# Kernel optimization log

Measured on AMD Instinct MI355X. Metric: run time of the kernel, lower is better.

## Reference

```python
import jax, jax.numpy as jnp
import numpy as np

B, C, H, W = 16, 256, 56, 56
HEADS, DHEAD = 8, 32
INNER = HEADS * DHEAD  # == C
BLOCK, HALO = 7, 3
WIN = BLOCK + 2 * HALO      # 13
REL = WIN                   # rel_size = block + 2*halo
HIDDEN = 4 * C
EPS = 1e-6
LS_INIT = 1e-6


def layernorm2d(x, w, b):
    # channels-first LayerNorm over C, x: (B,C,H,W)
    u = jnp.mean(x, axis=1, keepdims=True)
    s = jnp.mean((x - u) ** 2, axis=1, keepdims=True)
    xn = (x - u) * jax.lax.rsqrt(s + EPS)
    return w[None, :, None, None] * xn + b[None, :, None, None]


def rel_to_abs(x):
    # x: (b, l, 2r-1) -> (b, l, r)
    b, l, m = x.shape
    r = (m + 1) // 2
    x = jnp.pad(x, ((0, 0), (0, 0), (0, 1))).reshape(b, l * (m + 1))
    x = jnp.pad(x, ((0, 0), (0, m - l))).reshape(b, l + 1, m)
    return x[:, :l, -r:]


def relative_logits_1d(q, rel_k):
    # q: (b, h, w, d); rel_k: (2r-1, d) -> (b, h, r, w, r)
    b, h, w, _ = q.shape
    r = (rel_k.shape[0] + 1) // 2
    logits = jnp.einsum('bxyd,rd->bxyr', q, rel_k)
    logits = rel_to_abs(logits.reshape(b * h, w, -1)).reshape(b, h, w, r)
    return jnp.broadcast_to(logits[:, :, None], (b, h, r, w, r))


def rel_pos_bias(q, rel_h, rel_w):
    b = q.shape[0]
    r = (rel_w.shape[0] + 1) // 2
    q2 = q.reshape(b, BLOCK, BLOCK, DHEAD)
    lw = relative_logits_1d(q2, rel_w)                        # (b, x, i, y, j)
    lw = lw.transpose(0, 1, 3, 2, 4).reshape(b, BLOCK * BLOCK, r * r)
    lh = relative_logits_1d(q2.transpose(0, 2, 1, 3), rel_h)  # (b, y, i, x, j)
    lh = lh.transpose(0, 3, 1, 4, 2).reshape(b, BLOCK * BLOCK, r * r)
    return lw + lh


def halo_attention(x, wq, wkv, wo, bo, rel_h, rel_w):
    Bq, _, Hh, Ww = x.shape
    nh, nw = Hh // BLOCK, Ww // BLOCK
    nb = nh * nw
    # queries: non-overlapping blocks -> (B*nb, BLOCK^2, C)
    q_inp = x.reshape(Bq, C, nh, BLOCK, nw, BLOCK).transpose(0, 2, 4, 3, 5, 1)
    q_inp = q_inp.reshape(Bq * nb, BLOCK * BLOCK, C)
    # keys/values: overlapping haloed windows (like F.unfold with padding=HALO)
    xp = jnp.pad(x, ((0, 0), (0, 0), (HALO, HALO), (HALO, HALO)))
    rows = (jnp.arange(nh) * BLOCK)[:, None] + jnp.arange(WIN)
    cols = (jnp.arange(nw) * BLOCK)[:, None] + jnp.arange(WIN)
    kv = xp[:, :, rows][:, :, :, :, cols]
    kv = kv.transpose(0, 2, 4, 3, 5, 1).reshape(Bq * nb, WIN * WIN, C)
    q = q_inp @ wq.T
    k, v = jnp.split(kv @ wkv.T, 2, axis=-1)

    def split_heads(t):
        b2, n2, _ = t.shape
        return t.reshape(b2, n2, HEADS, DHEAD).transpose(0, 2, 1, 3).reshape(b2 * HEADS, n2, DHEAD)

    q, k, v = map(split_heads, (q, k, v))
    q = q * (DHEAD ** -0.5)
    sim = jnp.einsum('bid,bjd->bij', q, k) + rel_pos_bias(q, rel_h, rel_w)
    # mask out-of-bounds (zero-padded) halo positions
    onep = jnp.pad(jnp.ones((Hh, Ww), sim.dtype), ((HALO, HALO), (HALO, HALO)))
    m = (onep[rows][:, :, cols].transpose(0, 2, 1, 3).reshape(nb, WIN * WIN)) > 0
    sim = sim.reshape(Bq, nb, HEADS, BLOCK * BLOCK, WIN * WIN)
    sim = jnp.where(m[None, :, None, None, :], sim, -jnp.finfo(sim.dtype).max)
    sim = sim.reshape(Bq * nb * HEADS, BLOCK * BLOCK, WIN * WIN)
    attn = jax.nn.softmax(sim, axis=-1)
    out = jnp.einsum('bij,bjd->bid', attn, v)
    out = out.reshape(Bq * nb, HEADS, BLOCK * BLOCK, DHEAD).transpose(0, 2, 1, 3)
    out = out.reshape(Bq * nb, BLOCK * BLOCK, INNER) @ wo.T + bo
    out = out.reshape(Bq, nh, nw, BLOCK, BLOCK, C).transpose(0, 5, 1, 3, 2, 4)
    return out.reshape(Bq, C, Hh, Ww)


def _forward(x, ln1_w, ln1_b, ln2_w, ln2_b, wq, wkv, wo, bo, rel_h, rel_w,
             gamma1, gamma2, fc1_w, fc1_b, fc2_w, fc2_b):
    y = halo_attention(layernorm2d(x, ln1_w, ln1_b), wq, wkv, wo, bo, rel_h, rel_w)
    x = x + gamma1 * y  # drop_path = 0 -> identity
    z = layernorm2d(x, ln2_w, ln2_b).transpose(0, 2, 3, 1)  # NHWC
    z = jax.nn.gelu(z @ fc1_w.T + fc1_b, approximate=False)
    z = z @ fc2_w.T + fc2_b
    z = gamma2 * z
    return x + z.transpose(0, 3, 1, 2)


def setup_inputs() -> dict:
    key = jax.random.key(0)
    ks = jax.random.split(key, 8)
    n = lambda k, sh: jax.random.normal(k, sh, jnp.float32) * 0.02
    scale = DHEAD ** -0.5
    return dict(
        x=jax.random.normal(ks[0], (B, C, H, W), jnp.float32),
        ln1_w=jnp.ones((C,), jnp.float32), ln1_b=jnp.zeros((C,), jnp.float32),
        ln2_w=jnp.ones((C,), jnp.float32), ln2_b=jnp.zeros((C,), jnp.float32),
        wq=n(ks[1], (INNER, C)),
        wkv=n(ks[2], (2 * INNER, C)),
        wo=n(ks[3], (C, INNER)), bo=jnp.zeros((C,), jnp.float32),
        rel_h=jax.random.normal(ks[4], (2 * REL - 1, DHEAD), jnp.float32) * scale,
        rel_w=jax.random.normal(ks[5], (2 * REL - 1, DHEAD), jnp.float32) * scale,
        gamma1=jnp.full((1, C, 1, 1), LS_INIT, jnp.float32),
        gamma2=jnp.full((1, 1, 1, C), LS_INIT, jnp.float32),
        fc1_w=n(ks[6], (HIDDEN, C)), fc1_b=jnp.zeros((HIDDEN,), jnp.float32),
        fc2_w=n(ks[7], (C, HIDDEN)), fc2_b=jnp.zeros((C,), jnp.float32),
    )


def reference(x, ln1_w, ln1_b, ln2_w, ln2_b, wq, wkv, wo, bo, rel_h, rel_w,
              gamma1, gamma2, fc1_w, fc1_b, fc2_w, fc2_b):
    return _forward(x, ln1_w, ln1_b, ln2_w, ln2_b, wq, wkv, wo, bo, rel_h, rel_w,
                    gamma1, gamma2, fc1_w, fc1_b, fc2_w, fc2_b)
```

## Files before the change

### kernel.cpp

```cpp
#include <hip/hip_runtime.h>
#include <cmath>

#define DI __device__ __forceinline__

typedef unsigned short ushort_t;
typedef __attribute__((ext_vector_type(8))) short short8;
typedef __attribute__((ext_vector_type(8))) unsigned short ushort8;
typedef __attribute__((ext_vector_type(4))) unsigned short ushort4_t;
typedef __attribute__((ext_vector_type(4))) float floatx4;
typedef unsigned int u32;
typedef __attribute__((ext_vector_type(4))) u32 uintx4;

DI float bf2f(ushort_t u) {
    unsigned v = ((unsigned)u) << 16;
    float f;
    __builtin_memcpy(&f, &v, 4);
    return f;
}
DI ushort_t f2bf(float f) {
    unsigned u;
    __builtin_memcpy(&u, &f, 4);
    unsigned r = (u + 0x7FFFu + ((u >> 16) & 1u)) >> 16;
    return (ushort_t)r;
}
DI ushort_t f2bf_tr(float f) {
    unsigned u;
    __builtin_memcpy(&u, &f, 4);
    return (ushort_t)(u >> 16);
}
DI u32 pack2bf(float lo, float hi) {
    u32 a, b;
    __builtin_memcpy(&a, &lo, 4);
    __builtin_memcpy(&b, &hi, 4);
    return (a >> 16) | (b & 0xFFFF0000u);
}

DI void async_copy16(const ushort_t* gsrc, ushort_t* ldst) {
    auto gp = (const __attribute__((address_space(1))) u32*)gsrc;
    auto lp = (__attribute__((address_space(3))) u32*)ldst;
    __builtin_amdgcn_global_load_lds(gp, lp, 16, 0, 0);
}


__global__ void convert_all_kernel(const float* __restrict__ wq, const float* __restrict__ wkv,
                                   const float* __restrict__ wo, const float* __restrict__ fc1w,
                                   const float* __restrict__ fc2w, const float* __restrict__ relh,
                                   const float* __restrict__ relw,
                                   ushort_t* __restrict__ bqkv, ushort_t* __restrict__ woC,
                                   ushort_t* __restrict__ fc1C, ushort_t* __restrict__ fc2C,
                                   ushort_t* __restrict__ relC, ushort_t* __restrict__ boneB) {
    int i = blockIdx.x * 256 + threadIdx.x;
    if (i < 196608) { bqkv[i] = f2bf(i < 65536 ? wq[i] : wkv[i - 65536]); return; }
    i -= 196608;
    if (i < 65536) { woC[i] = f2bf(wo[i]); return; }
    i -= 65536;
    if (i < 262144) { fc1C[i] = f2bf(fc1w[i]); return; }
    i -= 262144;
    if (i < 262144) { fc2C[i] = f2bf(fc2w[i]); return; }
    i -= 262144;
    if (i < 800) { relC[i] = f2bf(relh[i]); return; }
    i -= 800;
    if (i < 800) { relC[800 + i] = f2bf(relw[i]); return; }
    i -= 800;
    if (i < 5632) {
        int j = i >> 5, k = i & 31;
        int kh = j / 13, kw = j - kh * 13;
        ushort_t v = 0;
        if (j < 169) {
            if (k == kh || k == 13 + kw) v = 0x3F80;
            if (k == 28 && kh < 3) v = 0x3F80;
            if (k == 29 && kh >= 10) v = 0x3F80;
            if (k == 30 && kw < 3) v = 0x3F80;
            if (k == 31 && kw >= 10) v = 0x3F80;
        } else {
            if (k == 27) v = 0x3F80;
        }
        boneB[i] = v;
    }
}

__global__ __launch_bounds__(256) void ln1_kernel(const float* __restrict__ x,
                                                  const float* __restrict__ w,
                                                  const float* __restrict__ bias,
                                                  ushort_t* __restrict__ t1,
                                                  float* __restrict__ xh) {
    __shared__ __align__(16) float lds[56 * 256];
    int b = blockIdx.x / 56, h = blockIdx.x % 56;
    int c = threadIdx.x;
    const float* row = x + (((size_t)(b * 256 + c) * 56 + h) * 56);
    floatx4 vals[14];
#pragma unroll
    for (int i = 0; i < 14; i++) vals[i] = *(const floatx4*)(row + i * 4);
#pragma unroll
    for (int i = 0; i < 14; i++)
#pragma unroll
        for (int e = 0; e < 4; e++) lds[(i * 4 + e) * 256 + c] = vals[i][e];
    __syncthreads();
    int wv = threadIdx.x >> 6, lane = threadIdx.x & 63;
    for (int p0 = 0; p0 < 14; p0++) {
        int p = wv * 14 + p0;
        float xv[4];
        float s = 0.f, q = 0.f;
#pragma unroll
        for (int j = 0; j < 4; j++) {
            xv[j] = lds[p * 256 + lane * 4 + j];
            s += xv[j];
            q += xv[j] * xv[j];
        }
#pragma unroll
        for (int off = 32; off; off >>= 1) {
            s += __shfl_xor(s, off);
            q += __shfl_xor(q, off);
        }
        float mean = s * (1.f / 256.f);
        float var = q * (1.f / 256.f) - mean * mean;
        float rstd = rsqrtf(var + 1e-6f);
        size_t token = ((size_t)b * 56 + h) * 56 + p;
        ushort4_t o4;
        floatx4 x4;
#pragma unroll
        for (int j = 0; j < 4; j++) {
            int cc = lane * 4 + j;
            o4[j] = f2bf_tr(w[cc] * ((xv[j] - mean) * rstd) + bias[cc]);
            x4[j] = xv[j];
        }
        *(ushort4_t*)(t1 + token * 256 + lane * 4) = o4;
        *(floatx4*)(xh + token * 256 + lane * 4) = x4;
    }
}

template <int EPI>
__global__ __launch_bounds__(256) void gemm_kernel(const ushort_t* __restrict__ A,
                                                   const ushort_t* __restrict__ Bw,
                                                   void* __restrict__ Cout, int K, int N,
                                                   const float* __restrict__ biasf,
                                                   const float* __restrict__ resf,
                                                   const float* __restrict__ gammaf) {
    __shared__ __align__(16) ushort_t As[2][128 * 32];
    __shared__ __align__(16) ushort_t Bs[2][128 * 32];
    int m0 = blockIdx.x * 128, n0 = blockIdx.y * 128;
    int t = threadIdx.x;
    int wave = t >> 6, lane = t & 63;
    int wm = (wave & 1) * 64, wn = (wave >> 1) * 64;
    int lr = lane & 15, quad = lane >> 4;
    floatx4 acc[4][4] = {};

    int srow = t >> 2, sc16 = t & 3;
    int srow1 = srow + 64;
    const ushort_t* Arow0 = A + (size_t)(m0 + srow) * K + sc16 * 8;
    const ushort_t* Arow1 = A + (size_t)(m0 + srow1) * K + sc16 * 8;
    const ushort_t* Brow0 = Bw + (size_t)(n0 + srow) * K + sc16 * 8;
    const ushort_t* Brow1 = Bw + (size_t)(n0 + srow1) * K + sc16 * 8;

    async_copy16(Arow0, &As[0][t * 8]);
    async_copy16(Brow0, &Bs[0][t * 8]);
    async_copy16(Arow1, &As[0][(t + 256) * 8]);
    async_copy16(Brow1, &Bs[0][(t + 256) * 8]);
    __syncthreads();

    int cur = 0;
    for (int k0 = 0; k0 < K; k0 += 32) {
        if (k0 + 32 < K) {
            int nk = k0 + 32;
            async_copy16(Arow0 + nk, &As[cur ^ 1][t * 8]);
            async_copy16(Brow0 + nk, &Bs[cur ^ 1][t * 8]);
            async_copy16(Arow1 + nk, &As[cur ^ 1][(t + 256) * 8]);
            async_copy16(Brow1 + nk, &Bs[cur ^ 1][(t + 256) * 8]);
        }
        short8 af[4], bf[4];
#pragma unroll
        for (int i = 0; i < 4; i++) af[i] = *(const short8*)(&As[cur][(wm + i * 16 + lr) * 32 + quad * 8]);
#pragma unroll
        for (int i = 0; i < 4; i++) bf[i] = *(const short8*)(&Bs[cur][(wn + i * 16 + lr) * 32 + quad * 8]);
#pragma unroll
        for (int i = 0; i < 4; i++)
#pragma unroll
            for (int j = 0; j < 4; j++)
                acc[i][j] = __builtin_amdgcn_mfma_f32_16x16x32_bf16(af[i], bf[j], acc[i][j], 0, 0, 0);
        __syncthreads();
        cur ^= 1;
    }
    const float qsc = (EPI == 3 && n0 < 256) ? 0.17677669529663687f : 1.0f;
#pragma unroll
    for (int i = 0; i < 4; i++)
#pragma unroll
        for (int j = 0; j < 4; j++)
#pragma unroll
            for (int r = 0; r < 4; r++) {
                int row = m0 + wm + i * 16 + quad * 4 + r;
                int col = n0 + wn + j * 16 + lr;
                float v = acc[i][j][r];
                if (EPI == 1) {
                    v = resf[(size_t)row * N + col] + gammaf[col] * (v + biasf[col]);
                    ((float*)Cout)[(size_t)row * N + col] = v;
                } else if (EPI == 2) {
                    v += biasf[col];
                    float s = __expf(-1.702f * v);
                    v = v * __builtin_amdgcn_rcpf(1.0f + s);
                    ((ushort_t*)Cout)[(size_t)row * N + col] = f2bf_tr(v);
                } else {
                    ((ushort_t*)Cout)[(size_t)row * N + col] = f2bf_tr(v * qsc);
                }
            }
}

__global__ __launch_bounds__(256, 4) void attn_kernel(const ushort_t* __restrict__ qkv,
                                                      const ushort_t* __restrict__ relh,
                                                      const ushort_t* __restrict__ relw,
                                                      const ushort_t* __restrict__ bone,
                                                      ushort_t* __restrict__ attnout) {
    __shared__ __align__(16) char smem[30208];
    ushort_t* Vt = (ushort_t*)smem;
    ushort_t* tblA = (ushort_t*)(smem + 12800);
    ushort_t* Ks = (ushort_t*)(smem + 16896);
    ushort_t* Ps = (ushort_t*)(smem + 16896);

    int wg = blockIdx.x;
    int head = wg & 7;
    int blk = (wg >> 3) & 63;
    int b = wg >> 9;
    int bh = blk >> 3, bw = blk & 7;
    int t = threadIdx.x;
    int wave = t >> 6, lane = t & 63;
    int lr = lane & 15, quad = lane >> 4;
    const int base_tok = b * 3136;

    short8 bbr[11];
#pragma unroll
    for (int nt = 0; nt < 11; nt++)
        bbr[nt] = *(const short8*)(bone + (nt * 16 + lr) * 32 + quad * 8);
    short8 bfg4[4];
#pragma unroll
    for (int ntile = 0; ntile < 4; ntile++) {
        int n = ntile * 16 + lr;
        int eff = (n < 50) ? n : 0;
        const ushort_t* rp = (eff < 25) ? (relh + eff * 32) : (relw + (eff - 25) * 32);
        bfg4[ntile] = *(const short8*)(rp + quad * 8);
    }
    short8 aq;
    {
        int qrow = wave * 16 + lr;
        int qx = qrow / 7, qy = qrow - qx * 7;
        int tok = min(base_tok + (bh * 7 + qx) * 56 + (bw * 7 + qy), 50175);
        aq = *(const short8*)(qkv + (size_t)tok * 768 + head * 32 + quad * 8);
    }

    ushort8 vv[3];
    int vrow[3], vcol[3];
#pragma unroll
    for (int it = 0; it < 3; it++) {
        int c = t + it * 256;
        bool act = (it < 2) || (t < 192);
        int j = c >> 2, ck = c & 3;
        int kh = j / 13, kw = j - kh * 13;
        int gh = bh * 7 + kh - 3, gw = bw * 7 + kw - 3;
        int tok = min(max(base_tok + gh * 56 + gw, 0), 50175);
        const ushort_t* src = qkv + (size_t)tok * 768 + head * 32 + ck * 8;
        if (act) {
            async_copy16(src + 256, Ks + c * 8);
            vv[it] = *(const ushort8*)(src + 512);
        }
        int nt = j >> 4, l2 = j & 15;
        vcol[it] = (nt >= 6) ? (96 + l2 * 6 + nt - 6) : (l2 * 6 + nt);
        vrow[it] = ck * 8;
    }
#pragma unroll
    for (int it = 0; it < 3; it++) {
        bool act = (it < 2) || (t < 192);
        if (act) {
#pragma unroll
            for (int e = 0; e < 8; e++) Vt[(vrow[it] + e) * 200 + vcol[it]] = vv[it][e];
        }
    }
#pragma unroll
    for (int i = 0; i < 2; i++) {
        int idx = t + i * 256;
        int row = idx >> 4, l2 = idx & 15;
        Vt[row * 200 + 96 + l2 * 6 + 5] = 0;
    }
    {
        const u32 NEG = 0xCE6Eu;
        bool himask = (t & 3) == 3;
        u32 e1 = himask ? (NEG << 16) : 0u;
        u32 e2m = himask ? ((bh == 0 ? NEG : 0u) | (bh == 7 ? NEG << 16 : 0u)) : 0u;
        u32 e3m = himask ? ((bw == 0 ? NEG : 0u) | (bw == 7 ? NEG << 16 : 0u)) : 0u;
        uintx4 ini = {0u, e1, e2m, e3m};
        *(uintx4*)(smem + 12800 + t * 16) = ini;
    }
    __syncthreads();

    floatx4 zero4 = {0.f, 0.f, 0.f, 0.f};

    int qx_r[4], qy_r[4];
#pragma unroll
    for (int r = 0; r < 4; r++) {
        int row = wave * 16 + quad * 4 + r;
        qx_r[r] = row / 7;
        qy_r[r] = row - qx_r[r] * 7;
    }

#pragma unroll
    for (int ntile = 0; ntile < 4; ntile++) {
        int n = ntile * 16 + lr;
        floatx4 cta = __builtin_amdgcn_mfma_f32_16x16x32_bf16(aq, bfg4[ntile], zero4, 0, 0, 0);
#pragma unroll
        for (int r = 0; r < 4; r++) {
            int slot = (n < 25) ? (n - 12 + qx_r[r]) : (n - 24 + qy_r[r]);
            bool ok = (n < 25) ? (slot >= 0 && slot <= 12)
                               : (n < 50 && slot >= 13 && slot <= 25);
            int ss = ok ? slot : 26;
            tblA[(wave * 16 + quad * 4 + r) * 32 + ss] = f2bf_tr(cta[r]);
        }
    }

    short8 afb = *(const short8*)(tblA + (wave * 16 + lr) * 32 + quad * 8);
    floatx4 sacc[11];
#pragma unroll
    for (int nt = 0; nt < 11; nt++) {
        short8 bk = *(const short8*)(Ks + (nt * 16 + lr) * 32 + quad * 8);
        floatx4 s0 = __builtin_amdgcn_mfma_f32_16x16x32_bf16(aq, bk, zero4, 0, 0, 0);
        sacc[nt] = __builtin_amdgcn_mfma_f32_16x16x32_bf16(afb, bbr[nt], s0, 0, 0, 0);
    }

    __syncthreads();

    u32 phi[4][3];
#pragma unroll
    for (int r = 0; r < 4; r++) {
        int qr2 = wave * 16 + quad * 4 + r;
        float eb[11];
#pragma unroll
        for (int nt = 0; nt < 11; nt++) eb[nt] = __expf(sacc[nt][r]);
        u32* prow = (u32*)(Ps + qr2 * 104 + lr * 6);
        prow[0] = pack2bf(eb[0], eb[1]);
        prow[1] = pack2bf(eb[2], eb[3]);
        prow[2] = pack2bf(eb[4], eb[5]);
        phi[r][0] = pack2bf(eb[6], eb[7]);
        phi[r][1] = pack2bf(eb[8], eb[9]);
        phi[r][2] = pack2bf(eb[10], 0.f);
    }

    short8 ones8;
#pragma unroll
    for (int e = 0; e < 8; e++) ones8[e] = (short)0x3F80;

    floatx4 oacc[2] = {zero4, zero4};
    floatx4 osum = zero4;
#pragma unroll
    for (int kk = 0; kk < 3; kk++) {
        int k0 = kk * 32;
        short8 ap = *(const short8*)(Ps + (wave * 16 + lr) * 104 + k0 + quad * 8);
#pragma unroll
        for (int n2 = 0; n2 < 2; n2++) {
            short8 bv = *(const short8*)(Vt + (n2 * 16 + lr) * 200 + k0 + quad * 8);
            oacc[n2] = __builtin_amdgcn_mfma_f32_16x16x32_bf16(ap, bv, oacc[n2], 0, 0, 0);
        }
        osum = __builtin_amdgcn_mfma_f32_16x16x32_bf16(ap, ones8, osum, 0, 0, 0);
    }
#pragma unroll
    for (int r = 0; r < 4; r++) {
        int qr2 = wave * 16 + quad * 4 + r;
        u32* prow = (u32*)(Ps + qr2 * 104 + lr * 6);
        prow[0] = phi[r][0];
        prow[1] = phi[r][1];
        prow[2] = phi[r][2];
    }
#pragma unroll
    for (int kk = 0; kk < 3; kk++) {
        int k0 = kk * 32;
        short8 ap = *(const short8*)(Ps + (wave * 16 + lr) * 104 + k0 + quad * 8);
#pragma unroll
        for (int n2 = 0; n2 < 2; n2++) {
            short8 bv = *(const short8*)(Vt + (n2 * 16 + lr) * 200 + 96 + k0 + quad * 8);
            oacc[n2] = __builtin_amdgcn_mfma_f32_16x16x32_bf16(ap, bv, oacc[n2], 0, 0, 0);
        }
        osum = __builtin_amdgcn_mfma_f32_16x16x32_bf16(ap, ones8, osum, 0, 0, 0);
    }

#pragma unroll
    for (int n2 = 0; n2 < 2; n2++)
#pragma unroll
        for (int r = 0; r < 4; r++) {
            int qr2 = wave * 16 + quad * 4 + r;
            if (qr2 < 49) {
                float inv = __builtin_amdgcn_rcpf(osum[r]);
                int qx = qr2 / 7, qy = qr2 - qx * 7;
                size_t tok = (size_t)base_tok + (bh * 7 + qx) * 56 + (bw * 7 + qy);
                attnout[tok * 256 + head * 32 + n2 * 16 + lr] = f2bf_tr(oacc[n2][r] * inv);
            }
        }
}

__global__ __launch_bounds__(256) void ln2_kernel(const float* __restrict__ xin,
                                                  const float* __restrict__ w,
                                                  const float* __restrict__ bias,
                                                  ushort_t* __restrict__ o) {
    int token = blockIdx.x * 4 + (threadIdx.x >> 6);
    int lane = threadIdx.x & 63;
    floatx4 v4 = *(const floatx4*)(xin + (size_t)token * 256 + lane * 4);
    float s = 0.f, q = 0.f;
#pragma unroll
    for (int i = 0; i < 4; i++) {
        s += v4[i];
        q += v4[i] * v4[i];
    }
#pragma unroll
    for (int off = 32; off; off >>= 1) {
        s += __shfl_xor(s, off);
        q += __shfl_xor(q, off);
    }
    float mean = s * (1.f / 256.f);
    float var = q * (1.f / 256.f) - mean * mean;
    float rstd = rsqrtf(var + 1e-6f);
    ushort4_t o4;
#pragma unroll
    for (int i = 0; i < 4; i++) {
        int c = lane * 4 + i;
        o4[i] = f2bf_tr(w[c] * ((v4[i] - mean) * rstd) + bias[c]);
    }
    *(ushort4_t*)(o + (size_t)token * 256 + lane * 4) = o4;
}

__global__ __launch_bounds__(256) void out_transpose_kernel(const float* __restrict__ s,
                                                            float* __restrict__ o) {
    __shared__ __align__(16) float lds[56 * 256];
    int b = blockIdx.x / 56, h = blockIdx.x % 56;
    const float* src = s + (((size_t)b * 56 + h) * 56) * 256;
    int t = threadIdx.x;
#pragma unroll
    for (int i = 0; i < 14; i++) {
        int chunk = i * 256 + t;
        *(floatx4*)(lds + chunk * 4) = *(const floatx4*)(src + chunk * 4);
    }
    __syncthreads();
    int c = t;
    float* dst = o + (((size_t)b * 256 + c) * 56 + h) * 56;
#pragma unroll
    for (int i = 0; i < 14; i++) {
        floatx4 v;
#pragma unroll
        for (int e = 0; e < 4; e++) v[e] = lds[(i * 4 + e) * 256 + c];
        *(floatx4*)(dst + i * 4) = v;
    }
}

extern "C" void kernel_launch(void* const* d_in, const int* in_sizes, int n_in,
                              void* d_out, int out_size, void* d_ws, size_t ws_size,
                              hipStream_t stream) {
    const float* x = (const float*)d_in[0];
    const float* ln1w = (const float*)d_in[1];
    const float* ln1b = (const float*)d_in[2];
    const float* ln2w = (const float*)d_in[3];
    const float* ln2b = (const float*)d_in[4];
    const float* wq = (const float*)d_in[5];
    const float* wkv = (const float*)d_in[6];
    const float* wo = (const float*)d_in[7];
    const float* bo = (const float*)d_in[8];
    const float* relh = (const float*)d_in[9];
    const float* relw = (const float*)d_in[10];
    const float* g1 = (const float*)d_in[11];
    const float* g2 = (const float*)d_in[12];
    const float* fc1w = (const float*)d_in[13];
    const float* fc1b = (const float*)d_in[14];
    const float* fc2w = (const float*)d_in[15];
    const float* fc2b = (const float*)d_in[16];
    float* out = (float*)d_out;

    char* ws = (char*)d_ws;
    float* xh = (float*)ws;
    float* x1 = xh;
    float* sbuf = xh;
    ushort_t* t1 = (ushort_t*)(ws + 51380224);
    ushort_t* attnb = t1;
    ushort_t* qkv = (ushort_t*)(ws + 77070336);
    ushort_t* t2 = qkv;
    ushort_t* hid = (ushort_t*)(ws + 77070336 + 25690112);
    ushort_t* wv_ = (ushort_t*)(ws + 154140672);
    ushort_t* bqkv = wv_;
    ushort_t* woC = wv_ + 196608;
    ushort_t* fc1C = woC + 65536;
    ushort_t* fc2C = fc1C + 262144;
    ushort_t* relC = fc2C + 262144;
    ushort_t* boneG = relC + 1600;

    convert_all_kernel<<<3101, 256, 0, stream>>>(wq, wkv, wo, fc1w, fc2w, relh, relw,
                                                 bqkv, woC, fc1C, fc2C, relC, boneG);
    ln1_kernel<<<896, 256, 0, stream>>>(x, ln1w, ln1b, t1, xh);
    gemm_kernel<3><<<dim3(392, 6), 256, 0, stream>>>(t1, bqkv, qkv, 256, 768, nullptr, nullptr, nullptr);
    attn_kernel<<<8192, 256, 0, stream>>>(qkv, relC, relC + 800, boneG, attnb);
    gemm_kernel<1><<<dim3(392, 2), 256, 0, stream>>>(attnb, woC, x1, 256, 256, bo, xh, g1);
    ln2_kernel<<<12544, 256, 0, stream>>>(x1, ln2w, ln2b, t2);
    const size_t CH = 25088;
    for (int c = 0; c < 2; c++) {
        gemm_kernel<2><<<dim3(196, 8), 256, 0, stream>>>(t2 + c * CH * 256, fc1C, hid, 256, 1024, fc1b, nullptr, nullptr);
        gemm_kernel<1><<<dim3(196, 2), 256, 0, stream>>>(hid, fc2C, sbuf + c * CH * 256, 1024, 256, fc2b, x1 + c * CH * 256, g2);
    }
    out_transpose_kernel<<<896, 256, 0, stream>>>(sbuf, out);
}
```

Baseline: 427.3 us.

## Fuse NCHW layout transforms into GEMM epilogues and remap block order

The output-projection GEMM now reads the residual directly from the NCHW input, so ln1 no longer writes a token-major fp32 copy. The final fc2 GEMM writes its result straight into NCHW output, which removes the separate transpose kernel and its full fp32 round trip. Workgroup indices are remapped so consecutive blocks are spread across eight groups, likely to match chiplet or L2 placement. The attention kernel's V-transpose row stride is padded from 200 to 204 to reduce LDS bank conflicts. In exchange, the epilogues gather a 4-row column strip from NCHW (stride 3136), which is less coalesced.

```diff
diff --git a/kernel.cpp b/kernel.cpp
--- a/kernel.cpp
+++ b/kernel.cpp
@@ -82,8 +82,7 @@
 __global__ __launch_bounds__(256) void ln1_kernel(const float* __restrict__ x,
                                                   const float* __restrict__ w,
                                                   const float* __restrict__ bias,
-                                                  ushort_t* __restrict__ t1,
-                                                  float* __restrict__ xh) {
+                                                  ushort_t* __restrict__ t1) {
     __shared__ __align__(16) float lds[56 * 256];
     int b = blockIdx.x / 56, h = blockIdx.x % 56;
     int c = threadIdx.x;
@@ -117,15 +116,12 @@
         float rstd = rsqrtf(var + 1e-6f);
         size_t token = ((size_t)b * 56 + h) * 56 + p;
         ushort4_t o4;
-        floatx4 x4;
 #pragma unroll
         for (int j = 0; j < 4; j++) {
             int cc = lane * 4 + j;
             o4[j] = f2bf_tr(w[cc] * ((xv[j] - mean) * rstd) + bias[cc]);
-            x4[j] = xv[j];
         }
         *(ushort4_t*)(t1 + token * 256 + lane * 4) = o4;
-        *(floatx4*)(xh + token * 256 + lane * 4) = x4;
     }
 }
 
@@ -135,10 +131,16 @@
                                                    void* __restrict__ Cout, int K, int N,
                                                    const float* __restrict__ biasf,
                                                    const float* __restrict__ resf,
-                                                   const float* __restrict__ gammaf) {
+                                                   const float* __restrict__ gammaf,
+                                                   int tok0) {
     __shared__ __align__(16) ushort_t As[2][128 * 32];
     __shared__ __align__(16) ushort_t Bs[2][128 * 32];
-    int m0 = blockIdx.x * 128, n0 = blockIdx.y * 128;
+    int gy = gridDim.y;
+    int lin = blockIdx.y * gridDim.x + blockIdx.x;
+    int chunk = (gridDim.x * gy) >> 3;
+    int wl = (lin & 7) * chunk + (lin >> 3);
+    int mt = wl / gy;
+    int m0 = mt * 128, n0 = (wl - mt * gy) * 128;
     int t = threadIdx.x;
     int wave = t >> 6, lane = t & 63;
     int wm = (wave & 1) * 64, wn = (wave >> 1) * 64;
@@ -184,24 +186,40 @@
 #pragma unroll
     for (int i = 0; i < 4; i++)
 #pragma unroll
-        for (int j = 0; j < 4; j++)
-#pragma unroll
-            for (int r = 0; r < 4; r++) {
-                int row = m0 + wm + i * 16 + quad * 4 + r;
-                int col = n0 + wn + j * 16 + lr;
-                float v = acc[i][j][r];
-                if (EPI == 1) {
-                    v = resf[(size_t)row * N + col] + gammaf[col] * (v + biasf[col]);
-                    ((float*)Cout)[(size_t)row * N + col] = v;
-                } else if (EPI == 2) {
-                    v += biasf[col];
+        for (int j = 0; j < 4; j++) {
+            int row0 = m0 + wm + i * 16 + quad * 4;
+            int col = n0 + wn + j * 16 + lr;
+            if (EPI == 4) {
+                int tokg = tok0 + row0;
+                int bb = tokg / 3136;
+                int rem = tokg - bb * 3136;
+                floatx4 ov;
+#pragma unroll
+                for (int r = 0; r < 4; r++)
+                    ov[r] = resf[(size_t)(row0 + r) * N + col] + gammaf[col] * (acc[i][j][r] + biasf[col]);
+                *(floatx4*)((float*)Cout + (size_t)(bb * 256 + col) * 3136 + rem) = ov;
+            } else if (EPI == 5) {
+                int bb = row0 / 3136;
+                int rem = row0 - bb * 3136;
+                floatx4 rx = *(const floatx4*)(resf + (size_t)(bb * 256 + col) * 3136 + rem);
+#pragma unroll
+                for (int r = 0; r < 4; r++)
+                    ((float*)Cout)[(size_t)(row0 + r) * N + col] =
+                        rx[r] + gammaf[col] * (acc[i][j][r] + biasf[col]);
+            } else if (EPI == 2) {
+#pragma unroll
+                for (int r = 0; r < 4; r++) {
+                    float v = acc[i][j][r] + biasf[col];
                     float s = __expf(-1.702f * v);
                     v = v * __builtin_amdgcn_rcpf(1.0f + s);
-                    ((ushort_t*)Cout)[(size_t)row * N + col] = f2bf_tr(v);
-                } else {
-                    ((ushort_t*)Cout)[(size_t)row * N + col] = f2bf_tr(v * qsc);
+                    ((ushort_t*)Cout)[(size_t)(row0 + r) * N + col] = f2bf_tr(v);
                 }
+            } else {
+#pragma unroll
+                for (int r = 0; r < 4; r++)
+                    ((ushort_t*)Cout)[(size_t)(row0 + r) * N + col] = f2bf_tr(acc[i][j][r] * qsc);
             }
+        }
 }
 
 __global__ __launch_bounds__(256, 4) void attn_kernel(const ushort_t* __restrict__ qkv,
@@ -209,11 +227,11 @@
                                                       const ushort_t* __restrict__ relw,
                                                       const ushort_t* __restrict__ bone,
                                                       ushort_t* __restrict__ attnout) {
-    __shared__ __align__(16) char smem[30208];
+    __shared__ __align__(16) char smem[30464];
     ushort_t* Vt = (ushort_t*)smem;
-    ushort_t* tblA = (ushort_t*)(smem + 12800);
-    ushort_t* Ks = (ushort_t*)(smem + 16896);
-    ushort_t* Ps = (ushort_t*)(smem + 16896);
+    ushort_t* tblA = (ushort_t*)(smem + 13056);
+    ushort_t* Ks = (ushort_t*)(smem + 17152);
+    ushort_t* Ps = (ushort_t*)(smem + 17152);
 
     int wg = blockIdx.x;
     int head = wg & 7;
@@ -269,14 +287,14 @@
         bool act = (it < 2) || (t < 192);
         if (act) {
 #pragma unroll
-            for (int e = 0; e < 8; e++) Vt[(vrow[it] + e) * 200 + vcol[it]] = vv[it][e];
+            for (int e = 0; e < 8; e++) Vt[(vrow[it] + e) * 204 + vcol[it]] = vv[it][e];
         }
     }
 #pragma unroll
     for (int i = 0; i < 2; i++) {
         int idx = t + i * 256;
         int row = idx >> 4, l2 = idx & 15;
-        Vt[row * 200 + 96 + l2 * 6 + 5] = 0;
+        Vt[row * 204 + 96 + l2 * 6 + 5] = 0;
     }
     {
         const u32 NEG = 0xCE6Eu;
@@ -285,7 +303,7 @@
         u32 e2m = himask ? ((bh == 0 ? NEG : 0u) | (bh == 7 ? NEG << 16 : 0u)) : 0u;
         u32 e3m = himask ? ((bw == 0 ? NEG : 0u) | (bw == 7 ? NEG << 16 : 0u)) : 0u;
         uintx4 ini = {0u, e1, e2m, e3m};
-        *(uintx4*)(smem + 12800 + t * 16) = ini;
+        *(uintx4*)(smem + 13056 + t * 16) = ini;
     }
     __syncthreads();
 
@@ -352,7 +370,7 @@
         short8 ap = *(const short8*)(Ps + (wave * 16 + lr) * 104 + k0 + quad * 8);
 #pragma unroll
         for (int n2 = 0; n2 < 2; n2++) {
-            short8 bv = *(const short8*)(Vt + (n2 * 16 + lr) * 200 + k0 + quad * 8);
+            short8 bv = *(const short8*)(Vt + (n2 * 16 + lr) * 204 + k0 + quad * 8);
             oacc[n2] = __builtin_amdgcn_mfma_f32_16x16x32_bf16(ap, bv, oacc[n2], 0, 0, 0);
         }
         osum = __builtin_amdgcn_mfma_f32_16x16x32_bf16(ap, ones8, osum, 0, 0, 0);
@@ -371,7 +389,7 @@
         short8 ap = *(const short8*)(Ps + (wave * 16 + lr) * 104 + k0 + quad * 8);
 #pragma unroll
         for (int n2 = 0; n2 < 2; n2++) {
-            short8 bv = *(const short8*)(Vt + (n2 * 16 + lr) * 200 + 96 + k0 + quad * 8);
+            short8 bv = *(const short8*)(Vt + (n2 * 16 + lr) * 204 + 96 + k0 + quad * 8);
             oacc[n2] = __builtin_amdgcn_mfma_f32_16x16x32_bf16(ap, bv, oacc[n2], 0, 0, 0);
         }
         osum = __builtin_amdgcn_mfma_f32_16x16x32_bf16(ap, ones8, osum, 0, 0, 0);
@@ -419,29 +437,6 @@
         o4[i] = f2bf_tr(w[c] * ((v4[i] - mean) * rstd) + bias[c]);
     }
     *(ushort4_t*)(o + (size_t)token * 256 + lane * 4) = o4;
-}
-
-__global__ __launch_bounds__(256) void out_transpose_kernel(const float* __restrict__ s,
-                                                            float* __restrict__ o) {
-    __shared__ __align__(16) float lds[56 * 256];
-    int b = blockIdx.x / 56, h = blockIdx.x % 56;
-    const float* src = s + (((size_t)b * 56 + h) * 56) * 256;
-    int t = threadIdx.x;
-#pragma unroll
-    for (int i = 0; i < 14; i++) {
-        int chunk = i * 256 + t;
-        *(floatx4*)(lds + chunk * 4) = *(const floatx4*)(src + chunk * 4);
-    }
-    __syncthreads();
-    int c = t;
-    float* dst = o + (((size_t)b * 256 + c) * 56 + h) * 56;
-#pragma unroll
-    for (int i = 0; i < 14; i++) {
-        floatx4 v;
-#pragma unroll
-        for (int e = 0; e < 4; e++) v[e] = lds[(i * 4 + e) * 256 + c];
-        *(floatx4*)(dst + i * 4) = v;
-    }
 }
 
 extern "C" void kernel_launch(void* const* d_in, const int* in_sizes, int n_in,
@@ -467,9 +462,7 @@
     float* out = (float*)d_out;
 
     char* ws = (char*)d_ws;
-    float* xh = (float*)ws;
-    float* x1 = xh;
-    float* sbuf = xh;
+    float* x1 = (float*)ws;
     ushort_t* t1 = (ushort_t*)(ws + 51380224);
     ushort_t* attnb = t1;
     ushort_t* qkv = (ushort_t*)(ws + 77070336);
@@ -485,15 +478,14 @@
 
     convert_all_kernel<<<3101, 256, 0, stream>>>(wq, wkv, wo, fc1w, fc2w, relh, relw,
                                                  bqkv, woC, fc1C, fc2C, relC, boneG);
-    ln1_kernel<<<896, 256, 0, stream>>>(x, ln1w, ln1b, t1, xh);
-    gemm_kernel<3><<<dim3(392, 6), 256, 0, stream>>>(t1, bqkv, qkv, 256, 768, nullptr, nullptr, nullptr);
+    ln1_kernel<<<896, 256, 0, stream>>>(x, ln1w, ln1b, t1);
+    gemm_kernel<3><<<dim3(392, 6), 256, 0, stream>>>(t1, bqkv, qkv, 256, 768, nullptr, nullptr, nullptr, 0);
     attn_kernel<<<8192, 256, 0, stream>>>(qkv, relC, relC + 800, boneG, attnb);
-    gemm_kernel<1><<<dim3(392, 2), 256, 0, stream>>>(attnb, woC, x1, 256, 256, bo, xh, g1);
+    gemm_kernel<5><<<dim3(392, 2), 256, 0, stream>>>(attnb, woC, x1, 256, 256, bo, x, g1, 0);
     ln2_kernel<<<12544, 256, 0, stream>>>(x1, ln2w, ln2b, t2);
     const size_t CH = 25088;
     for (int c = 0; c < 2; c++) {
-        gemm_kernel<2><<<dim3(196, 8), 256, 0, stream>>>(t2 + c * CH * 256, fc1C, hid, 256, 1024, fc1b, nullptr, nullptr);
-        gemm_kernel<1><<<dim3(196, 2), 256, 0, stream>>>(hid, fc2C, sbuf + c * CH * 256, 1024, 256, fc2b, x1 + c * CH * 256, g2);
-    }
-    out_transpose_kernel<<<896, 256, 0, stream>>>(sbuf, out);
-}
+        gemm_kernel<2><<<dim3(196, 8), 256, 0, stream>>>(t2 + c * CH * 256, fc1C, hid, 256, 1024, fc1b, nullptr, nullptr, 0);
+        gemm_kernel<4><<<dim3(196, 2), 256, 0, stream>>>(hid, fc2C, out, 1024, 256, fc2b, x1 + c * CH * 256, g2, (int)(c * CH));
+    }
+}
```

After: 402.9 us. 5.7% less time.
